# Kernel optimization log

Hardware: AMD Instinct MI355X
Metric: run time of the kernel (lower is better)

Reference implementation:

```python
import jax, jax.numpy as jnp
import numpy as np

W_GLOBAL, W_SOFT, W_HARD = 0.2, 0.3, 0.5
GAMMA, ALPHA = 2.0, 0.25
MIN_TEMP, MAX_TEMP = 0.01, 100.0
EPS = 1e-12


def _l2norm(x, axis):
    n = jnp.sqrt(jnp.sum(x * x, axis=axis, keepdims=True))
    return x / jnp.maximum(n, EPS)


def _focal_ce(logits, labels):
    # torch F.cross_entropy with label_smoothing=ALPHA, then focal modulation
    log_p = jax.nn.log_softmax(logits, axis=-1)           # (B, K)
    nll = -jnp.take_along_axis(log_p, labels[:, None], axis=-1)[:, 0]
    smooth = -jnp.mean(log_p, axis=-1)
    ce = (1.0 - ALPHA) * nll + ALPHA * smooth
    pt = jnp.exp(-ce)
    return jnp.mean((1.0 - pt) ** GAMMA * ce)


def setup_inputs() -> dict:
    key = jax.random.key(0)
    k1, k2, k3 = jax.random.split(key, 3)
    B, C, N = 256, 512, 512
    yolo_feats = jax.random.normal(k1, (B, C, N), dtype=jnp.float32)
    clip_feats = jax.random.normal(k2, (B, C), dtype=jnp.float32)
    logit_scale = jax.random.uniform(k3, (1,), dtype=jnp.float32) * 2.0 + 2.0
    return {"yolo_feats": yolo_feats, "clip_feats": clip_feats, "logit_scale": logit_scale}


def reference(yolo_feats, clip_feats, logit_scale):
    yolo_feats = _l2norm(yolo_feats, axis=1)              # (B, C, N)
    clip_feats = _l2norm(clip_feats, axis=1)              # (B, C)
    scale = jnp.clip(jnp.exp(logit_scale), MIN_TEMP, MAX_TEMP)  # (1,)
    B = yolo_feats.shape[0]
    labels = jnp.arange(B, dtype=jnp.int32)

    # global branch
    yolo_global = _l2norm(jnp.mean(yolo_feats, axis=2), axis=1)   # (B, C)
    sim_global = (yolo_global @ clip_feats.T) * scale             # (B, B)
    loss_global = 0.5 * (_focal_ce(sim_global, labels) + _focal_ce(sim_global.T, labels))

    # dense spatial similarity map (B, N, K=B)
    sim_map = jnp.einsum('bcn,kc->bnk', yolo_feats, clip_feats) * scale

    sim_soft = jax.nn.logsumexp(sim_map, axis=1)                  # (B, B)
    loss_soft = 0.5 * (_focal_ce(sim_soft, labels) + _focal_ce(sim_soft.T, labels))

    sim_hard = jnp.max(sim_map, axis=1)                           # (B, B)
    loss_hard = 0.5 * (_focal_ce(sim_hard, labels) + _focal_ce(sim_hard.T, labels))

    return W_GLOBAL * loss_global + W_SOFT * loss_soft + W_HARD * loss_hard
```

## Files before the change

### kernel.cpp

```cpp
#include <hip/hip_runtime.h>
#include <hip/hip_bf16.h>
#include <math.h>

constexpr int B = 256;
constexpr int C = 512;
constexpr int N = 512;
constexpr int K = 256;
constexpr int NWIN = 8;
constexpr int NSLOT = B * NWIN;

constexpr size_t OFF_CLIPNB = 0;
constexpr size_t OFF_U      = OFF_CLIPNB + (size_t)B*C/2;
constexpr size_t OFF_PM     = OFF_U      + (size_t)NSLOT*C;
constexpr size_t OFF_PS     = OFF_PM     + (size_t)NSLOT*K;
constexpr size_t OFF_PH     = OFF_PS     + (size_t)NSLOT*K;
constexpr size_t OFF_PG     = OFF_PH     + (size_t)NSLOT*K;
constexpr size_t OFF_SGLOB  = OFF_PG     + (size_t)NSLOT*K;
constexpr size_t OFF_SSOFT  = OFF_SGLOB  + (size_t)B*K;
constexpr size_t OFF_SHARD  = OFF_SSOFT  + (size_t)B*K;
constexpr size_t OFF_MISC   = OFF_SHARD  + (size_t)B*K;

typedef __attribute__((ext_vector_type(8))) short short8;
typedef __attribute__((ext_vector_type(4))) float f32x4;

__device__ __forceinline__ float wave_reduce_sum(float v) {
  #pragma unroll
  for (int off = 32; off > 0; off >>= 1) v += __shfl_xor(v, off, 64);
  return v;
}
__device__ __forceinline__ float wave_reduce_max(float v) {
  #pragma unroll
  for (int off = 32; off > 0; off >>= 1) v = fmaxf(v, __shfl_xor(v, off, 64));
  return v;
}
__device__ __forceinline__ unsigned int bf16_rne(float x) {
  unsigned int u = __builtin_bit_cast(unsigned int, x);
  return (u + 0x7FFFu + ((u >> 16) & 1u)) >> 16;
}
__device__ __forceinline__ unsigned int pk2(float x, float y) {
  union { __hip_bfloat162 h; unsigned int u; } cv;
  cv.h = __float22bfloat162_rn(make_float2(x, y));
  return cv.u;
}

__global__ void k_misc(const float* __restrict__ ls, float* __restrict__ misc) {
  int t = threadIdx.x;
  if (t == 0) misc[0] = fminf(fmaxf(expf(ls[0]), 0.01f), 100.0f);
  if (t >= 1 && t < 7) misc[t] = 0.0f;
}

__global__ __launch_bounds__(256) void k_rownorm(const float* __restrict__ src,
                                                 unsigned short* __restrict__ dst_bf) {
  int b = blockIdx.x, t = threadIdx.x;
  float x0 = src[(size_t)b * C + t];
  float x1 = src[(size_t)b * C + t + 256];
  __shared__ float red[4];
  float w = wave_reduce_sum(x0 * x0 + x1 * x1);
  if ((t & 63) == 0) red[t >> 6] = w;
  __syncthreads();
  float tot = red[0] + red[1] + red[2] + red[3];
  float r = 1.0f / fmaxf(sqrtf(tot), 1e-12f);
  dst_bf[(size_t)b * C + t] = (unsigned short)bf16_rne(x0 * r);
  dst_bf[(size_t)b * C + t + 256] = (unsigned short)bf16_rne(x1 * r);
}

__global__ __launch_bounds__(256, 2) void k_main_mfma(
    const float* __restrict__ yolo,
    const unsigned short* __restrict__ clipnb,
    const float* __restrict__ misc,
    float* __restrict__ U,
    float* __restrict__ PM2, float* __restrict__ PS2,
    float* __restrict__ PH2, float* __restrict__ PG2) {
  int bw = blockIdx.x;
  int b = bw >> 3, win = bw & 7;
  int n0 = win * 64;
  int t = threadIdx.x;
  int w = t >> 6, lane = t & 63;
  int quad = lane >> 4, col = lane & 15;

  __shared__ unsigned int xl[64 * 256];
  __shared__ float ssqb[16 * 64];
  __shared__ float invt[64];

  const float scale = misc[0];
  const float* ybase = yolo + (size_t)b * C * N + n0;

  int nf = t & 15;
  int cp0 = t >> 4;
  unsigned int rotv = (8u * (nf & 3) + 4u * (unsigned)(nf >> 2)) & 31u;

  f32x4 acc[4][4];
  #pragma unroll
  for (int kt = 0; kt < 4; kt++)
    #pragma unroll
    for (int nt = 0; nt < 4; nt++) {
      f32x4 z = {0.f, 0.f, 0.f, 0.f};
      acc[kt][nt] = z;
    }

  float4 ssq4 = {0.f, 0.f, 0.f, 0.f};

  float4 Ya[2][2], Yb[2][2];
  #pragma unroll
  for (int q = 0; q < 2; q++)
    #pragma unroll
    for (int p = 0; p < 2; p++) {
      const float* pa = ybase + (size_t)(q * 64 + 2 * (cp0 + 16 * p)) * N + 4 * nf;
      Ya[q][p] = *(const float4*)pa;
      Yb[q][p] = *(const float4*)(pa + N);
    }

  #pragma unroll
  for (int cc = 0; cc < 8; cc++) {
    int c0 = cc * 64;
    int par = cc & 1;

    #pragma unroll
    for (int p = 0; p < 2; p++) {
      float4 a = Ya[par][p], bb = Yb[par][p];
      ssq4.x += a.x * a.x + bb.x * bb.x;
      ssq4.y += a.y * a.y + bb.y * bb.y;
      ssq4.z += a.z * a.z + bb.z * bb.z;
      ssq4.w += a.w * a.w + bb.w * bb.w;
      unsigned int pos = ((unsigned)(cp0 + 16 * p) + rotv) & 31u;
      int base0 = (4 * nf) * 256 + cc * 32;
      xl[base0 + pos]        = pk2(a.x, bb.x);
      xl[base0 + 256 + pos]  = pk2(a.y, bb.y);
      xl[base0 + 512 + pos]  = pk2(a.z, bb.z);
      xl[base0 + 768 + pos]  = pk2(a.w, bb.w);
    }

    if (cc < 6) {
      #pragma unroll
      for (int p = 0; p < 2; p++) {
        const float* pa =
            ybase + (size_t)((cc + 2) * 64 + 2 * (cp0 + 16 * p)) * N + 4 * nf;
        Ya[par][p] = *(const float4*)pa;
        Yb[par][p] = *(const float4*)(pa + N);
      }
    }

    short8 afr[4][2];
    #pragma unroll
    for (int kt = 0; kt < 4; kt++)
      #pragma unroll
      for (int s = 0; s < 2; s++) {
        const unsigned short* ap =
            clipnb + (size_t)(64 * w + 16 * kt + col) * C + c0 + 32 * s + 8 * quad;
        union { uint4 u; short8 v; } fa;
        fa.u = *(const uint4*)ap;
        afr[kt][s] = fa.v;
      }

    asm volatile("s_waitcnt lgkmcnt(0)" ::: "memory");
    __builtin_amdgcn_s_barrier();

    #pragma unroll
    for (int s = 0; s < 2; s++) {
      #pragma unroll
      for (int nt = 0; nt < 4; nt++) {
        int n = 16 * nt + col;
        unsigned int pos =
            (unsigned)(16 * s + 4 * quad + 8 * (col >> 2) + 4 * nt) & 31u;
        union { uint4 u; short8 v; } fb;
        fb.u = *(const uint4*)&xl[n * 256 + cc * 32 + pos];
        #pragma unroll
        for (int kt = 0; kt < 4; kt++)
          acc[kt][nt] = __builtin_amdgcn_mfma_f32_16x16x32_bf16(
              afr[kt][s], fb.v, acc[kt][nt], 0, 0, 0);
      }
    }
  }

  *(float4*)&ssqb[cp0 * 64 + 4 * nf] = ssq4;
  __syncthreads();
  if (t < 64) {
    float s = 0.f;
    #pragma unroll
    for (int g = 0; g < 16; g++) s += ssqb[g * 64 + t];
    invt[t] = 1.0f / fmaxf(sqrtf(s), 1e-12f);
  }
  __syncthreads();

  {
    int chU = t >> 5, cl = t & 31;
    float u0 = 0.f, u1 = 0.f;
    #pragma unroll
    for (int n = 0; n < 64; n++) {
      unsigned int d =
          xl[n * 256 + chU * 32 + ((cl + 8 * ((n >> 2) & 3) + 4 * (n >> 4)) & 31)];
      float iv = invt[n];
      union { unsigned int u; float f; } lo, hi;
      lo.u = d << 16;
      hi.u = d & 0xFFFF0000u;
      u0 += lo.f * iv;
      u1 += hi.f * iv;
    }
    *(float2*)&U[(size_t)bw * C + 2 * t] = make_float2(u0, u1);
  }

  float invn[4];
  #pragma unroll
  for (int nt = 0; nt < 4; nt++) invn[nt] = invt[16 * nt + col];
  #pragma unroll
  for (int kt = 0; kt < 4; kt++)
    #pragma unroll
    for (int r = 0; r < 4; r++) {
      float mm = -1e30f, ss = 0.f, hh = -1e30f, gg = 0.f;
      #pragma unroll
      for (int nt = 0; nt < 4; nt++) {
        float vu = acc[kt][nt][r] * invn[nt];
        gg += vu;
        float v = vu * scale;
        hh = fmaxf(hh, v);
        float M = fmaxf(mm, v);
        ss = ss * __expf(mm - M) + __expf(v - M);
        mm = M;
      }
      #pragma unroll
      for (int o = 1; o < 16; o <<= 1) {
        float mo = __shfl_xor(mm, o, 64);
        float so = __shfl_xor(ss, o, 64);
        float ho = __shfl_xor(hh, o, 64);
        float go = __shfl_xor(gg, o, 64);
        float M = fmaxf(mm, mo);
        ss = ss * __expf(mm - M) + so * __expf(mo - M);
        mm = M;
        hh = fmaxf(hh, ho);
        gg += go;
      }
      if (col == 0) {
        int k = 64 * w + 16 * kt + 4 * quad + r;
        size_t a = (size_t)bw * 256 + k;
        PM2[a] = mm; PS2[a] = ss; PH2[a] = hh; PG2[a] = gg;
      }
    }
}

__global__ __launch_bounds__(256) void k_post(
    const float* __restrict__ U, const float* __restrict__ PG2,
    const float* __restrict__ PM2, const float* __restrict__ PS2,
    const float* __restrict__ PH2, const float* __restrict__ misc,
    float* __restrict__ Sglob, float* __restrict__ Ssoft,
    float* __restrict__ Shard) {
  int bI = blockIdx.x;
  int t = threadIdx.x;
  __shared__ float red[4];
  __shared__ float gnS;
  float sq = 0.f;
  #pragma unroll
  for (int half = 0; half < 2; half++) {
    int c = t + 256 * half;
    float u = 0.f;
    #pragma unroll
    for (int j = 0; j < 8; j++) u += U[((size_t)bI * 8 + j) * C + c];
    sq += u * u;
  }
  float wsum = wave_reduce_sum(sq);
  if ((t & 63) == 0) red[t >> 6] = wsum;
  __syncthreads();
  if (t == 0) {
    float s = red[0] + red[1] + red[2] + red[3];
    gnS = fmaxf(sqrtf(s) * (1.0f / (float)N), 1e-12f);
  }
  __syncthreads();
  float gn = gnS;
  int k = t;
  size_t p0 = (size_t)bI * 8 * 256 + k;
  float g = 0.f;
  #pragma unroll
  for (int j = 0; j < 8; j++) g += PG2[p0 + j * 256];
  Sglob[(size_t)bI * K + k] = misc[0] * g * (1.0f / (float)N) / gn;
  float M = -1e30f;
  #pragma unroll
  for (int j = 0; j < 8; j++) M = fmaxf(M, PM2[p0 + j * 256]);
  float S = 0.f;
  #pragma unroll
  for (int j = 0; j < 8; j++) S += PS2[p0 + j * 256] * __expf(PM2[p0 + j * 256] - M);
  Ssoft[(size_t)bI * K + k] = M + __logf(S);
  float H = -1e30f;
  #pragma unroll
  for (int j = 0; j < 8; j++) H = fmaxf(H, PH2[p0 + j * 256]);
  Shard[(size_t)bI * K + k] = H;
}

__global__ __launch_bounds__(256) void k_focal(const float* __restrict__ Sglob,
                                               const float* __restrict__ Ssoft,
                                               const float* __restrict__ Shard,
                                               float* __restrict__ misc) {
  int job = blockIdx.y;
  int i = blockIdx.x;
  int t = threadIdx.x;
  const float* M = job < 2 ? Sglob : (job < 4 ? Ssoft : Shard);
  float v = (job & 1) ? M[(size_t)t * K + i] : M[(size_t)i * K + t];
  __shared__ float red[4];
  float mx = wave_reduce_max(v);
  if ((t & 63) == 0) red[t >> 6] = mx;
  __syncthreads();
  mx = fmaxf(fmaxf(red[0], red[1]), fmaxf(red[2], red[3]));
  __syncthreads();
  float sv = wave_reduce_sum(v);
  if ((t & 63) == 0) red[t >> 6] = sv;
  __syncthreads();
  float sumv = red[0] + red[1] + red[2] + red[3];
  __syncthreads();
  float se = wave_reduce_sum(expf(v - mx));
  if ((t & 63) == 0) red[t >> 6] = se;
  __syncthreads();
  if (t == 0) {
    float sumexp = red[0] + red[1] + red[2] + red[3];
    float logZ = mx + logf(sumexp);
    float diag = M[(size_t)i * K + i];
    float nll = logZ - diag;
    float smooth = logZ - sumv * (1.0f / 256.0f);
    float ce = 0.75f * nll + 0.25f * smooth;
    float pt = expf(-ce);
    float fo = (1.0f - pt) * (1.0f - pt) * ce;
    atomicAdd(&misc[1 + job], fo);
  }
}

__global__ void k_finish(const float* __restrict__ misc, float* __restrict__ out) {
  float lg = misc[1] + misc[2];
  float ls = misc[3] + misc[4];
  float lh = misc[5] + misc[6];
  out[0] = (0.2f * lg + 0.3f * ls + 0.5f * lh) * 0.5f * (1.0f / 256.0f);
}

extern "C" void kernel_launch(void* const* d_in, const int* in_sizes, int n_in,
                              void* d_out, int out_size, void* d_ws, size_t ws_size,
                              hipStream_t stream) {
  const float* yolo = (const float*)d_in[0];
  const float* clip = (const float*)d_in[1];
  const float* ls   = (const float*)d_in[2];
  float* out = (float*)d_out;
  float* ws = (float*)d_ws;
  unsigned short* clipnb = (unsigned short*)(ws + OFF_CLIPNB);
  float* U     = ws + OFF_U;
  float* PM2   = ws + OFF_PM;
  float* PS2   = ws + OFF_PS;
  float* PH2   = ws + OFF_PH;
  float* PG2   = ws + OFF_PG;
  float* Sglob = ws + OFF_SGLOB;
  float* Ssoft = ws + OFF_SSOFT;
  float* Shard = ws + OFF_SHARD;
  float* misc  = ws + OFF_MISC;

  k_misc<<<1, 64, 0, stream>>>(ls, misc);
  k_rownorm<<<256, 256, 0, stream>>>(clip, clipnb);
  k_main_mfma<<<NSLOT, 256, 0, stream>>>(yolo, clipnb, misc, U,
                                         PM2, PS2, PH2, PG2);
  k_post<<<256, 256, 0, stream>>>(U, PG2, PM2, PS2, PH2, misc,
                                  Sglob, Ssoft, Shard);
  k_focal<<<dim3(256, 6), 256, 0, stream>>>(Sglob, Ssoft, Shard, misc);
  k_finish<<<1, 1, 0, stream>>>(misc, out);
}
```

Baseline: 430.0 us.

## Double main kernel block to 512 threads and fold misc kernel into rownorm

The main MFMA kernel now runs 512 threads per block. Each of the 8 waves covers 32 clip rows instead of 64, and each thread stages half as much yolo data per chunk. The U column-sum is split across two thread halves and combined through shared memory. Separately, the scale/misc initialisation kernel is merged into the rownorm kernel to save one launch. The aim is more waves in flight to hide global-load latency and fewer accumulator registers per thread, at the cost of an extra barrier and more shared-memory traffic per block.

```diff
diff --git a/kernel.cpp b/kernel.cpp
--- a/kernel.cpp
+++ b/kernel.cpp
@@ -43,15 +43,15 @@
   return cv.u;
 }
 
-__global__ void k_misc(const float* __restrict__ ls, float* __restrict__ misc) {
-  int t = threadIdx.x;
-  if (t == 0) misc[0] = fminf(fmaxf(expf(ls[0]), 0.01f), 100.0f);
-  if (t >= 1 && t < 7) misc[t] = 0.0f;
-}
-
 __global__ __launch_bounds__(256) void k_rownorm(const float* __restrict__ src,
-                                                 unsigned short* __restrict__ dst_bf) {
+                                                 const float* __restrict__ ls,
+                                                 unsigned short* __restrict__ dst_bf,
+                                                 float* __restrict__ misc) {
   int b = blockIdx.x, t = threadIdx.x;
+  if (b == 0 && t < 7) {
+    if (t == 0) misc[0] = fminf(fmaxf(expf(ls[0]), 0.01f), 100.0f);
+    else misc[t] = 0.0f;
+  }
   float x0 = src[(size_t)b * C + t];
   float x1 = src[(size_t)b * C + t + 256];
   __shared__ float red[4];
@@ -64,7 +64,7 @@
   dst_bf[(size_t)b * C + t + 256] = (unsigned short)bf16_rne(x1 * r);
 }
 
-__global__ __launch_bounds__(256, 2) void k_main_mfma(
+__global__ __launch_bounds__(512, 4) void k_main_mfma(
     const float* __restrict__ yolo,
     const unsigned short* __restrict__ clipnb,
     const float* __restrict__ misc,
@@ -79,19 +79,19 @@
   int quad = lane >> 4, col = lane & 15;
 
   __shared__ unsigned int xl[64 * 256];
-  __shared__ float ssqb[16 * 64];
+  __shared__ float ssqb[32 * 64];
   __shared__ float invt[64];
 
   const float scale = misc[0];
   const float* ybase = yolo + (size_t)b * C * N + n0;
 
   int nf = t & 15;
-  int cp0 = t >> 4;
+  int cp = t >> 4;
   unsigned int rotv = (8u * (nf & 3) + 4u * (unsigned)(nf >> 2)) & 31u;
 
-  f32x4 acc[4][4];
-  #pragma unroll
-  for (int kt = 0; kt < 4; kt++)
+  f32x4 acc[2][4];
+  #pragma unroll
+  for (int kt = 0; kt < 2; kt++)
     #pragma unroll
     for (int nt = 0; nt < 4; nt++) {
       f32x4 z = {0.f, 0.f, 0.f, 0.f};
@@ -100,29 +100,26 @@
 
   float4 ssq4 = {0.f, 0.f, 0.f, 0.f};
 
-  float4 Ya[2][2], Yb[2][2];
-  #pragma unroll
-  for (int q = 0; q < 2; q++)
-    #pragma unroll
-    for (int p = 0; p < 2; p++) {
-      const float* pa = ybase + (size_t)(q * 64 + 2 * (cp0 + 16 * p)) * N + 4 * nf;
-      Ya[q][p] = *(const float4*)pa;
-      Yb[q][p] = *(const float4*)(pa + N);
-    }
+  float4 Ya[2], Yb[2];
+  #pragma unroll
+  for (int q = 0; q < 2; q++) {
+    const float* pa = ybase + (size_t)(q * 64 + 2 * cp) * N + 4 * nf;
+    Ya[q] = *(const float4*)pa;
+    Yb[q] = *(const float4*)(pa + N);
+  }
 
   #pragma unroll
   for (int cc = 0; cc < 8; cc++) {
     int c0 = cc * 64;
     int par = cc & 1;
 
-    #pragma unroll
-    for (int p = 0; p < 2; p++) {
-      float4 a = Ya[par][p], bb = Yb[par][p];
+    {
+      float4 a = Ya[par], bb = Yb[par];
       ssq4.x += a.x * a.x + bb.x * bb.x;
       ssq4.y += a.y * a.y + bb.y * bb.y;
       ssq4.z += a.z * a.z + bb.z * bb.z;
       ssq4.w += a.w * a.w + bb.w * bb.w;
-      unsigned int pos = ((unsigned)(cp0 + 16 * p) + rotv) & 31u;
+      unsigned int pos = ((unsigned)cp + rotv) & 31u;
       int base0 = (4 * nf) * 256 + cc * 32;
       xl[base0 + pos]        = pk2(a.x, bb.x);
       xl[base0 + 256 + pos]  = pk2(a.y, bb.y);
@@ -131,22 +128,18 @@
     }
 
     if (cc < 6) {
-      #pragma unroll
-      for (int p = 0; p < 2; p++) {
-        const float* pa =
-            ybase + (size_t)((cc + 2) * 64 + 2 * (cp0 + 16 * p)) * N + 4 * nf;
-        Ya[par][p] = *(const float4*)pa;
-        Yb[par][p] = *(const float4*)(pa + N);
-      }
-    }
-
-    short8 afr[4][2];
-    #pragma unroll
-    for (int kt = 0; kt < 4; kt++)
+      const float* pa = ybase + (size_t)((cc + 2) * 64 + 2 * cp) * N + 4 * nf;
+      Ya[par] = *(const float4*)pa;
+      Yb[par] = *(const float4*)(pa + N);
+    }
+
+    short8 afr[2][2];
+    #pragma unroll
+    for (int kt = 0; kt < 2; kt++)
       #pragma unroll
       for (int s = 0; s < 2; s++) {
         const unsigned short* ap =
-            clipnb + (size_t)(64 * w + 16 * kt + col) * C + c0 + 32 * s + 8 * quad;
+            clipnb + (size_t)(32 * w + 16 * kt + col) * C + c0 + 32 * s + 8 * quad;
         union { uint4 u; short8 v; } fa;
         fa.u = *(const uint4*)ap;
         afr[kt][s] = fa.v;
@@ -165,30 +158,32 @@
         union { uint4 u; short8 v; } fb;
         fb.u = *(const uint4*)&xl[n * 256 + cc * 32 + pos];
         #pragma unroll
-        for (int kt = 0; kt < 4; kt++)
+        for (int kt = 0; kt < 2; kt++)
           acc[kt][nt] = __builtin_amdgcn_mfma_f32_16x16x32_bf16(
               afr[kt][s], fb.v, acc[kt][nt], 0, 0, 0);
       }
     }
   }
 
-  *(float4*)&ssqb[cp0 * 64 + 4 * nf] = ssq4;
+  *(float4*)&ssqb[cp * 64 + 4 * nf] = ssq4;
   __syncthreads();
   if (t < 64) {
     float s = 0.f;
     #pragma unroll
-    for (int g = 0; g < 16; g++) s += ssqb[g * 64 + t];
+    for (int g = 0; g < 32; g++) s += ssqb[g * 64 + t];
     invt[t] = 1.0f / fmaxf(sqrtf(s), 1e-12f);
   }
   __syncthreads();
 
   {
-    int chU = t >> 5, cl = t & 31;
+    int th = t & 255, nh = t >> 8;
+    int ccU = th >> 5, clU = th & 31;
     float u0 = 0.f, u1 = 0.f;
     #pragma unroll
-    for (int n = 0; n < 64; n++) {
+    for (int nn = 0; nn < 32; nn++) {
+      int n = nh * 32 + nn;
       unsigned int d =
-          xl[n * 256 + chU * 32 + ((cl + 8 * ((n >> 2) & 3) + 4 * (n >> 4)) & 31)];
+          xl[n * 256 + ccU * 32 + ((clU + 8 * ((n >> 2) & 3) + 4 * (n >> 4)) & 31)];
       float iv = invt[n];
       union { unsigned int u; float f; } lo, hi;
       lo.u = d << 16;
@@ -196,6 +191,13 @@
       u0 += lo.f * iv;
       u1 += hi.f * iv;
     }
+    ssqb[nh * 512 + th * 2]     = u0;
+    ssqb[nh * 512 + th * 2 + 1] = u1;
+  }
+  __syncthreads();
+  if (t < 256) {
+    float u0 = ssqb[t * 2]     + ssqb[512 + t * 2];
+    float u1 = ssqb[t * 2 + 1] + ssqb[512 + t * 2 + 1];
     *(float2*)&U[(size_t)bw * C + 2 * t] = make_float2(u0, u1);
   }
 
@@ -203,7 +205,7 @@
   #pragma unroll
   for (int nt = 0; nt < 4; nt++) invn[nt] = invt[16 * nt + col];
   #pragma unroll
-  for (int kt = 0; kt < 4; kt++)
+  for (int kt = 0; kt < 2; kt++)
     #pragma unroll
     for (int r = 0; r < 4; r++) {
       float mm = -1e30f, ss = 0.f, hh = -1e30f, gg = 0.f;
@@ -230,7 +232,7 @@
         gg += go;
       }
       if (col == 0) {
-        int k = 64 * w + 16 * kt + 4 * quad + r;
+        int k = 32 * w + 16 * kt + 4 * quad + r;
         size_t a = (size_t)bw * 256 + k;
         PM2[a] = mm; PS2[a] = ss; PH2[a] = hh; PG2[a] = gg;
       }
@@ -346,9 +348,8 @@
   float* Shard = ws + OFF_SHARD;
   float* misc  = ws + OFF_MISC;
 
-  k_misc<<<1, 64, 0, stream>>>(ls, misc);
-  k_rownorm<<<256, 256, 0, stream>>>(clip, clipnb);
-  k_main_mfma<<<NSLOT, 256, 0, stream>>>(yolo, clipnb, misc, U,
+  k_rownorm<<<256, 256, 0, stream>>>(clip, ls, clipnb, misc);
+  k_main_mfma<<<NSLOT, 512, 0, stream>>>(yolo, clipnb, misc, U,
                                          PM2, PS2, PH2, PG2);
   k_post<<<256, 256, 0, stream>>>(U, PG2, PM2, PS2, PH2, misc,
                                   Sglob, Ssoft, Shard);
```

Result: faster. 416.6 us (-3.1%).
